# Kernel tuning notes

Measured on AMD Instinct MI355X. Metric: run time of the kernel, lower is better.

## Reference

```python
import jax, jax.numpy as jnp
import numpy as np

H, D, E, C, F = 12, 64, 768, 512, 3072  # heads, kq_dim, emb_dim, context_dim, mlp_hid
EPS = 1e-5
SCALE = 1.0 / float(np.sqrt(D))


def setup_inputs() -> dict:
    key = jax.random.key(0)
    ks = jax.random.split(key, 12)
    rn = lambda k, s: jax.random.normal(k, s, dtype=jnp.float32) * 0.02
    z = lambda s: jnp.zeros(s, jnp.float32)
    o = lambda s: jnp.ones(s, jnp.float32)
    return {
        "emb": jax.random.normal(ks[0], (8, 1024, E), dtype=jnp.float32),
        "context": jax.random.normal(ks[1], (8, 256, C), dtype=jnp.float32),
        # self-attention (qkv_bias=False, value_up has bias)
        "sa_wq": rn(ks[2], (E, H * D)), "sa_wk": rn(ks[3], (E, H * D)),
        "sa_wv": rn(ks[4], (E, H * D)), "sa_wo": rn(ks[5], (H * D, E)), "sa_wo_b": z((E,)),
        "sa_qn_g": o((D,)), "sa_qn_b": z((D,)), "sa_kn_g": o((D,)), "sa_kn_b": z((D,)),
        # cross-attention
        "ca_wq": rn(ks[6], (E, H * D)), "ca_wk": rn(ks[7], (C, H * D)),
        "ca_wv": rn(ks[8], (C, H * D)), "ca_wo": rn(ks[9], (H * D, E)), "ca_wo_b": z((E,)),
        "ca_qn_g": o((D,)), "ca_qn_b": z((D,)), "ca_kn_g": o((D,)), "ca_kn_b": z((D,)),
        # MLP
        "mlp_w1": rn(ks[10], (E, F)), "mlp_b1": z((F,)),
        "mlp_w2": rn(ks[11], (F, E)), "mlp_b2": z((E,)),
        # block LayerNorms
        "ln1_g": o((E,)), "ln1_b": z((E,)),
        "ln2_g": o((E,)), "ln2_b": z((E,)),
        "ln3_g": o((E,)), "ln3_b": z((E,)),
    }


def _ln(x, g, b):
    m = jnp.mean(x, axis=-1, keepdims=True)
    v = jnp.mean(jnp.square(x - m), axis=-1, keepdims=True)
    return (x - m) / jnp.sqrt(v + EPS) * g + b


def _heads(x):  # [B,S,H*D] -> [B,H,S,D]
    B, S = x.shape[:2]
    return x.reshape(B, S, H, D).transpose(0, 2, 1, 3)


def _merge(x):  # [B,H,S,D] -> [B,S,H*D]
    B, h, S, d = x.shape
    return x.transpose(0, 2, 1, 3).reshape(B, S, h * d)


def _attn(qx, kvx, wq, wk, wv, wo, wo_b, qg, qb, kg, kb):
    q = _ln(_heads(qx @ wq), qg, qb)   # per-head QK-LayerNorm
    k = _ln(_heads(kvx @ wk), kg, kb)
    v = _heads(kvx @ wv)
    a = jax.nn.softmax(jnp.einsum('bhqd,bhkd->bhqk', q, k) * SCALE, axis=-1)
    return _merge(jnp.einsum('bhqk,bhkd->bhqd', a, v)) @ wo + wo_b


def reference(emb, context,
              sa_wq, sa_wk, sa_wv, sa_wo, sa_wo_b, sa_qn_g, sa_qn_b, sa_kn_g, sa_kn_b,
              ca_wq, ca_wk, ca_wv, ca_wo, ca_wo_b, ca_qn_g, ca_qn_b, ca_kn_g, ca_kn_b,
              mlp_w1, mlp_b1, mlp_w2, mlp_b2,
              ln1_g, ln1_b, ln2_g, ln2_b, ln3_g, ln3_b):
    # MultiHeadAttention.forward returns value + emb, and the block adds emb again
    sa = _attn(emb, emb, sa_wq, sa_wk, sa_wv, sa_wo, sa_wo_b,
               sa_qn_g, sa_qn_b, sa_kn_g, sa_kn_b)
    x = _ln(sa + emb + emb, ln1_g, ln1_b)  # faithful double residual
    ca = _attn(x, context, ca_wq, ca_wk, ca_wv, ca_wo, ca_wo_b,
               ca_qn_g, ca_qn_b, ca_kn_g, ca_kn_b)
    x = _ln(x + ca, ln2_g, ln2_b)
    x = jax.nn.gelu(x @ mlp_w1 + mlp_b1, approximate=False) @ mlp_w2 + mlp_b2
    return _ln(x, ln3_g, ln3_b)  # note: no residual around MLP in the original
```

## Files before the change

kernel.cpp:

```cpp
#include <hip/hip_runtime.h>
#include <hip/hip_bf16.h>
#include <math.h>

#define NH 12
#define HD 64
#define ED 768
#define CD 512
#define FD 3072
#define BB 8
#define SS 1024
#define TT 256
#define LN_EPS 1e-5f
#define ATT_SCALE 0.125f
#define QSC_LOG2E 0.1803368801111204f
#define P_M0 11.55f
#define TOT_R 6291456

typedef __attribute__((ext_vector_type(8))) __bf16 bf16x8;
typedef __attribute__((ext_vector_type(4))) __bf16 bf16x4;
typedef __attribute__((ext_vector_type(4))) float f32x4;

typedef const __attribute__((address_space(1))) void* gas1_t;
typedef __attribute__((address_space(3))) void* las3_t;

__device__ __forceinline__ void gl16(const void* g, void* l) {
  __builtin_amdgcn_global_load_lds((gas1_t)g, (las3_t)l, 16, 0, 0);
}

template <int N>
__device__ __forceinline__ void vm_wait() {
  if constexpr (N == 0) asm volatile("s_waitcnt vmcnt(0)" ::: "memory");
  else if constexpr (N == 3) asm volatile("s_waitcnt vmcnt(3)" ::: "memory");
  else if constexpr (N == 4) asm volatile("s_waitcnt vmcnt(4)" ::: "memory");
  else if constexpr (N == 6) asm volatile("s_waitcnt vmcnt(6)" ::: "memory");
  else if constexpr (N == 8) asm volatile("s_waitcnt vmcnt(8)" ::: "memory");
}

__device__ __forceinline__ ushort f2bf(float f) {
  union { __bf16 b; ushort u; } c;
  c.b = (__bf16)f;
  return c.u;
}

__device__ __forceinline__ float gelu_fast(float c) {
  const float x2 = c * c;
  const float ex = __builtin_amdgcn_exp2f(c * (-2.3022084f - 0.10294325f * x2));
  return c * __builtin_amdgcn_rcpf(1.0f + ex);
}

__device__ __forceinline__ bf16x8 frag64(const ushort (*T)[64], int row, int q8) {
  return *(const bf16x8*)((const char*)T + row * 128 + ((q8 ^ (row & 7)) << 4));
}

__device__ __forceinline__ bf16x8 frag32(const ushort (*T)[32], int row, int g) {
  return *(const bf16x8*)((const char*)T + row * 64 + ((g ^ ((row >> 1) & 3)) << 4));
}

struct CvtPack {
  const float* src[12];
  ushort* dst[12];
  int kd[12];
  int nd[12];
  int off[13];
};

__global__ __launch_bounds__(256) void cvt_all(CvtPack P) {
  __shared__ float t[32][33];
  const int flat = blockIdx.x;
  int j = 0;
  while (j < 11 && flat >= P.off[j + 1]) ++j;
  const int rel = flat - P.off[j];
  if (P.nd[j] == 0) {
    const int i = rel * 256 + threadIdx.x;
    if (i < P.kd[j]) {
      float4 v = ((const float4*)P.src[j])[i];
      ((ushort4*)P.dst[j])[i] =
          make_ushort4(f2bf(v.x), f2bf(v.y), f2bf(v.z), f2bf(v.w));
    }
    return;
  }
  const int Kd = P.kd[j], Nd = P.nd[j];
  const int ntx = Nd >> 5;
  const int n0 = (rel % ntx) * 32, k0 = (rel / ntx) * 32;
  const float* W = P.src[j];
  ushort* WT = P.dst[j];
  const int tx = threadIdx.x & 31, ty = threadIdx.x >> 5;
#pragma unroll
  for (int r = 0; r < 4; ++r)
    t[ty + 8 * r][tx] = W[(size_t)(k0 + ty + 8 * r) * Nd + n0 + tx];
  __syncthreads();
#pragma unroll
  for (int r = 0; r < 4; ++r)
    WT[(size_t)(n0 + ty + 8 * r) * Kd + k0 + tx] = f2bf(t[tx][ty + 8 * r]);
}

template <int MODE, int BM>
__global__ __launch_bounds__(256, 3) void mfma_gemm(
    const ushort* __restrict__ A, const ushort* __restrict__ Wt,
    const float* __restrict__ bias, void* __restrict__ outp,
    void* __restrict__ outp2, int M, int N, int Kstride, int Klen, int sshift,
    const float* __restrict__ qg, const float* __restrict__ qb,
    const float* __restrict__ kg, const float* __restrict__ kb,
    int t_q, int t_k, int t_v) {
  constexpr int MI = BM / 32;
  constexpr int LPS = BM / 64 + 2;
  __shared__ ushort As[3][BM][32];
  __shared__ ushort Bs[3][128][32];
  const int tid = threadIdx.x;
  const int m0 = blockIdx.x * BM, n0 = blockIdx.y * 128;
  const int kz = blockIdx.z;
  const ushort* Ab = A + (size_t)kz * Klen;
  const ushort* Wb = Wt + (size_t)kz * Klen;
  void* op = kz ? outp2 : outp;
  const int lane = tid & 63;
  const int wr = ((tid >> 6) >> 1) * (BM / 2), wc = ((tid >> 6) & 1) * 64;
  const int l15 = lane & 15, g = lane >> 4;
  f32x4 acc[MI][4] = {};

  auto stage = [&](int bi, int kt) {
#pragma unroll
    for (int p = 0; p < BM / 64; ++p) {
      const int fq = p * 256 + tid;
      const int row = fq >> 2, q = fq & 3;
      const int kc = 8 * (q ^ ((row >> 1) & 3));
      gl16(&Ab[(size_t)(m0 + row) * Kstride + kt + kc], (char*)As[bi] + fq * 16);
    }
#pragma unroll
    for (int p = 0; p < 2; ++p) {
      const int fq = p * 256 + tid;
      const int row = fq >> 2, q = fq & 3;
      const int kc = 8 * (q ^ ((row >> 1) & 3));
      gl16(&Wb[(size_t)(n0 + row) * Kstride + kt + kc], (char*)Bs[bi] + fq * 16);
    }
  };

  const int nst = Klen >> 5;
  stage(0, 0);
  stage(1, 32);
  int cb = 0;
  for (int step = 0; step < nst; ++step) {
    if (step + 2 < nst) {
      int pb = cb + 2; if (pb >= 3) pb -= 3;
      stage(pb, (step + 2) * 32);
    }
    const int rem = nst - 1 - step;
    if (rem >= 2) vm_wait<2 * LPS>();
    else if (rem == 1) vm_wait<LPS>();
    else vm_wait<0>();
    __builtin_amdgcn_s_barrier();
    asm volatile("" ::: "memory");
    bf16x8 af[MI], bfv[4];
#pragma unroll
    for (int i = 0; i < MI; ++i) af[i] = frag32(As[cb], wr + i * 16 + l15, g);
#pragma unroll
    for (int j = 0; j < 4; ++j) bfv[j] = frag32(Bs[cb], wc + j * 16 + l15, g);
#pragma unroll
    for (int i = 0; i < MI; ++i)
#pragma unroll
      for (int j = 0; j < 4; ++j)
        acc[i][j] = __builtin_amdgcn_mfma_f32_16x16x32_bf16(af[i], bfv[j],
                                                            acc[i][j], 0, 0, 0);
    asm volatile("" ::: "memory");
    __builtin_amdgcn_s_barrier();
    if (++cb >= 3) cb = 0;
  }

  if (MODE == 2) {
    ushort* out = (ushort*)op;
    const int Stok = 1 << sshift, smask = Stok - 1;
    const int ht0 = (n0 + wc) >> 6;
    const int t = ht0 / NH, h = ht0 - t * NH;
    const bool isq = (t == t_q), isk = (t == t_k);
    if (isq || isk) {
      const float* gg = isq ? qg : kg;
      const float* bb = isq ? qb : kb;
      const float osc = isq ? QSC_LOG2E : 1.0f;
      float gv[4], bv[4];
#pragma unroll
      for (int j = 0; j < 4; ++j) {
        gv[j] = gg[j * 16 + l15];
        bv[j] = bb[j * 16 + l15];
      }
#pragma unroll
      for (int i = 0; i < MI; ++i)
#pragma unroll
        for (int r = 0; r < 4; ++r) {
          float s = acc[i][0][r] + acc[i][1][r] + acc[i][2][r] + acc[i][3][r];
          float sq = acc[i][0][r] * acc[i][0][r] + acc[i][1][r] * acc[i][1][r] +
                     acc[i][2][r] * acc[i][2][r] + acc[i][3][r] * acc[i][3][r];
          s += __shfl_xor(s, 1);  sq += __shfl_xor(sq, 1);
          s += __shfl_xor(s, 2);  sq += __shfl_xor(sq, 2);
          s += __shfl_xor(s, 4);  sq += __shfl_xor(sq, 4);
          s += __shfl_xor(s, 8);  sq += __shfl_xor(sq, 8);
          const float mean = s * (1.0f / 64.0f);
          const float var = sq * (1.0f / 64.0f) - mean * mean;
          const float rs = rsqrtf(fmaxf(var, 0.0f) + LN_EPS);
#pragma unroll
          for (int j = 0; j < 4; ++j)
            acc[i][j][r] = ((acc[i][j][r] - mean) * rs * gv[j] + bv[j]) * osc;
        }
    }
    if (t == t_v) {
#pragma unroll
      for (int i = 0; i < MI; ++i) {
        const int row = m0 + wr + i * 16 + g * 4;
        const int b = row >> sshift, s2 = row & smask;
        ushort* obase =
            out + (size_t)t * TOT_R + (((size_t)b * NH + h) * 64) * Stok + s2;
#pragma unroll
        for (int j = 0; j < 4; ++j) {
          const int d = j * 16 + l15;
          ushort4 pk = make_ushort4(f2bf(acc[i][j][0]), f2bf(acc[i][j][1]),
                                    f2bf(acc[i][j][2]), f2bf(acc[i][j][3]));
          *(ushort4*)&obase[(size_t)d * Stok] = pk;
        }
      }
    } else {
#pragma unroll
      for (int i = 0; i < MI; ++i)
#pragma unroll
        for (int r = 0; r < 4; ++r) {
          const int row = m0 + wr + i * 16 + g * 4 + r;
          const int b = row >> sshift, s2 = row & smask;
          ushort* orow =
              out + (size_t)t * TOT_R + (((size_t)b * NH + h) * Stok + s2) * 64;
#pragma unroll
          for (int j = 0; j < 4; ++j) orow[j * 16 + l15] = f2bf(acc[i][j][r]);
        }
    }
  } else {
#pragma unroll
    for (int i = 0; i < MI; ++i) {
#pragma unroll
      for (int j = 0; j < 4; ++j) {
        const int gc = n0 + wc + j * 16 + l15;
        const float bv = bias ? bias[gc] : 0.0f;
#pragma unroll
        for (int r = 0; r < 4; ++r) {
          const int row = m0 + wr + i * 16 + g * 4 + r;
          float c = acc[i][j][r] + bv;
          if (MODE == 1) {
            c = gelu_fast(c);
            ((ushort*)op)[(size_t)row * N + gc] = f2bf(c);
          } else {
            ((float*)op)[(size_t)row * N + gc] = c;
          }
        }
      }
    }
  }
}

__global__ __launch_bounds__(512) void flash_mfma(
    const ushort* __restrict__ Q, const ushort* __restrict__ K,
    const ushort* __restrict__ V, ushort* __restrict__ out, int Tkv) {
  __shared__ ushort Ks[2][64][64];
  __shared__ ushort Vt[2][80][64];
  __shared__ ushort Ps[8][16][64];
  const int bh = blockIdx.x;
  const int b = bh / NH, h = bh % NH;
  const int qt = blockIdx.y;
  const int tid = threadIdx.x;
  const int w = tid >> 6, lane = tid & 63;
  const int l15 = lane & 15, g = lane >> 4;
  const int srow = tid >> 3;
  const int q8s = tid & 7;
  const int skc = 8 * (q8s ^ (srow & 7));
  const int kperm = 4 * (srow & 15) + (srow >> 4);

  const ushort* Qb = Q + ((size_t)bh * SS + qt * 256) * 64;
  const ushort* Kb = K + (size_t)bh * Tkv * 64;
  const ushort* Vb = V + (size_t)bh * Tkv * 64;

  gl16(&Kb[(size_t)kperm * 64 + skc], (char*)Ks[0] + tid * 16);
  gl16(&Vb[(size_t)srow * Tkv + skc], (char*)Vt[0] + tid * 16);

  if (tid < 256) {
    const int bi = tid >> 7, rq = tid & 127;
    const uint4 ov = make_uint4(0x3F803F80u, 0x3F803F80u, 0x3F803F80u, 0x3F803F80u);
    *(uint4*)((char*)Vt[bi] + (64 + (rq >> 3)) * 128 + ((rq & 7) << 4)) = ov;
  }

  const ushort* qr0 = Qb + (w * 32 + l15) * 64;
  const bf16x8 qf00 = *(const bf16x8*)&qr0[g * 8];
  const bf16x8 qf01 = *(const bf16x8*)&qr0[32 + g * 8];
  const bf16x8 qf10 = *(const bf16x8*)&qr0[16 * 64 + g * 8];
  const bf16x8 qf11 = *(const bf16x8*)&qr0[16 * 64 + 32 + g * 8];
  __syncthreads();

  f32x4 oa[2][5] = {};
  const int pwofs = ((((l15 >> 1) ^ ((g * 4) & 7)) << 4) | ((l15 & 1) << 3));

  const int nch = Tkv >> 6;
  int cur = 0;
  for (int ci = 0; ci < nch; ++ci) {
    if (ci + 1 < nch) {
      const int cnx = (ci + 1) << 6;
      const int nxt = cur ^ 1;
      gl16(&Kb[(size_t)(cnx + kperm) * 64 + skc], (char*)Ks[nxt] + tid * 16);
      gl16(&Vb[(size_t)srow * Tkv + cnx + skc], (char*)Vt[nxt] + tid * 16);
    }

    f32x4 s[2][4] = {};
    __builtin_amdgcn_s_setprio(1);
#pragma unroll
    for (int kb = 0; kb < 4; ++kb) {
      bf16x8 kf0 = frag64(Ks[cur], kb * 16 + l15, g);
      bf16x8 kf1 = frag64(Ks[cur], kb * 16 + l15, 4 + g);
      s[0][kb] = __builtin_amdgcn_mfma_f32_16x16x32_bf16(qf00, kf0, s[0][kb], 0, 0, 0);
      s[0][kb] = __builtin_amdgcn_mfma_f32_16x16x32_bf16(qf01, kf1, s[0][kb], 0, 0, 0);
      s[1][kb] = __builtin_amdgcn_mfma_f32_16x16x32_bf16(qf10, kf0, s[1][kb], 0, 0, 0);
      s[1][kb] = __builtin_amdgcn_mfma_f32_16x16x32_bf16(qf11, kf1, s[1][kb], 0, 0, 0);
    }
    __builtin_amdgcn_s_setprio(0);

    bf16x8 pfr[2][2];
#pragma unroll
    for (int sub = 0; sub < 2; ++sub) {
#pragma unroll
      for (int r = 0; r < 4; ++r) {
        bf16x4 pk;
#pragma unroll
        for (int kbv = 0; kbv < 4; ++kbv)
          pk[kbv] = (__bf16)__builtin_amdgcn_exp2f(s[sub][kbv][r] - P_M0);
        *(bf16x4*)((char*)Ps[w] + (g * 4 + r) * 128 + (pwofs ^ ((r & 7) << 4))) = pk;
      }
      pfr[sub][0] = frag64(Ps[w], l15, g);
      pfr[sub][1] = frag64(Ps[w], l15, 4 + g);
    }

    __builtin_amdgcn_s_setprio(1);
#pragma unroll
    for (int jd = 0; jd < 5; ++jd) {
      const int d = jd * 16 + l15;
      bf16x8 vf0 = frag64(Vt[cur], d, g);
      bf16x8 vf1 = frag64(Vt[cur], d, 4 + g);
      oa[0][jd] = __builtin_amdgcn_mfma_f32_16x16x32_bf16(pfr[0][0], vf0, oa[0][jd], 0, 0, 0);
      oa[0][jd] = __builtin_amdgcn_mfma_f32_16x16x32_bf16(pfr[0][1], vf1, oa[0][jd], 0, 0, 0);
      oa[1][jd] = __builtin_amdgcn_mfma_f32_16x16x32_bf16(pfr[1][0], vf0, oa[1][jd], 0, 0, 0);
      oa[1][jd] = __builtin_amdgcn_mfma_f32_16x16x32_bf16(pfr[1][1], vf1, oa[1][jd], 0, 0, 0);
    }
    __builtin_amdgcn_s_setprio(0);

    __syncthreads();
    cur ^= 1;
  }

#pragma unroll
  for (int sub = 0; sub < 2; ++sub)
#pragma unroll
    for (int r = 0; r < 4; ++r) {
      const int row = qt * 256 + w * 32 + sub * 16 + g * 4 + r;
      const float inv = 1.0f / oa[sub][4][r];
#pragma unroll
      for (int jd = 0; jd < 4; ++jd)
        out[((size_t)b * SS + row) * ED + h * 64 + jd * 16 + l15] =
            f2bf(oa[sub][jd][r] * inv);
    }
}

__global__ __launch_bounds__(256) void add_ln(
    const float* __restrict__ a1, const float* __restrict__ a2,
    const float* __restrict__ bsrc, float alpha,
    const float* __restrict__ cbias,
    const float* __restrict__ g, const float* __restrict__ bt,
    float* __restrict__ outf, ushort* __restrict__ outb) {
  const int row = blockIdx.x * 4 + (threadIdx.x >> 6);
  const int lane = threadIdx.x & 63;
  const size_t base = (size_t)row * ED;
  float4 x[3];
#pragma unroll
  for (int p = 0; p < 3; ++p) {
    const int idx = p * 256 + lane * 4;
    x[p] = *(const float4*)&a1[base + idx];
    if (a2) {
      float4 v = *(const float4*)&a2[base + idx];
      x[p].x += v.x; x[p].y += v.y; x[p].z += v.z; x[p].w += v.w;
    }
    if (bsrc) {
      float4 bv = *(const float4*)&bsrc[base + idx];
      x[p].x += alpha * bv.x;
      x[p].y += alpha * bv.y;
      x[p].z += alpha * bv.z;
      x[p].w += alpha * bv.w;
    }
    if (cbias) {
      float4 cv = *(const float4*)&cbias[idx];
      x[p].x += cv.x; x[p].y += cv.y; x[p].z += cv.z; x[p].w += cv.w;
    }
  }
  float s = 0.f;
#pragma unroll
  for (int p = 0; p < 3; ++p) s += x[p].x + x[p].y + x[p].z + x[p].w;
  for (int off = 32; off; off >>= 1) s += __shfl_xor(s, off);
  const float mean = s * (1.0f / 768.0f);
  float v = 0.f;
#pragma unroll
  for (int p = 0; p < 3; ++p) {
    float d0 = x[p].x - mean, d1 = x[p].y - mean;
    float d2 = x[p].z - mean, d3 = x[p].w - mean;
    v += d0 * d0 + d1 * d1 + d2 * d2 + d3 * d3;
  }
  for (int off = 32; off; off >>= 1) v += __shfl_xor(v, off);
  const float rs = rsqrtf(v * (1.0f / 768.0f) + LN_EPS);
#pragma unroll
  for (int p = 0; p < 3; ++p) {
    const int idx = p * 256 + lane * 4;
    const float4 gv = *(const float4*)&g[idx];
    const float4 bb = *(const float4*)&bt[idx];
    const float y0 = (x[p].x - mean) * rs * gv.x + bb.x;
    const float y1 = (x[p].y - mean) * rs * gv.y + bb.y;
    const float y2 = (x[p].z - mean) * rs * gv.z + bb.z;
    const float y3 = (x[p].w - mean) * rs * gv.w + bb.w;
    if (outf) *(float4*)&outf[base + idx] = make_float4(y0, y1, y2, y3);
    if (outb)
      *(ushort4*)&outb[base + idx] =
          make_ushort4(f2bf(y0), f2bf(y1), f2bf(y2), f2bf(y3));
  }
}

extern "C" void kernel_launch(void* const* d_in, const int* in_sizes, int n_in,
                              void* d_out, int out_size, void* d_ws,
                              size_t ws_size, hipStream_t stream) {
  (void)in_sizes; (void)n_in; (void)out_size; (void)ws_size;
  const float* emb     = (const float*)d_in[0];
  const float* context = (const float*)d_in[1];
  const float* sa_wq = (const float*)d_in[2];
  const float* sa_wk = (const float*)d_in[3];
  const float* sa_wv = (const float*)d_in[4];
  const float* sa_wo = (const float*)d_in[5];
  const float* sa_wo_b = (const float*)d_in[6];
  const float* sa_qn_g = (const float*)d_in[7];
  const float* sa_qn_b = (const float*)d_in[8];
  const float* sa_kn_g = (const float*)d_in[9];
  const float* sa_kn_b = (const float*)d_in[10];
  const float* ca_wq = (const float*)d_in[11];
  const float* ca_wk = (const float*)d_in[12];
  const float* ca_wv = (const float*)d_in[13];
  const float* ca_wo = (const float*)d_in[14];
  const float* ca_wo_b = (const float*)d_in[15];
  const float* ca_qn_g = (const float*)d_in[16];
  const float* ca_qn_b = (const float*)d_in[17];
  const float* ca_kn_g = (const float*)d_in[18];
  const float* ca_kn_b = (const float*)d_in[19];
  const float* mlp_w1 = (const float*)d_in[20];
  const float* mlp_b1 = (const float*)d_in[21];
  const float* mlp_w2 = (const float*)d_in[22];
  const float* mlp_b2 = (const float*)d_in[23];
  const float* ln1_g = (const float*)d_in[24];
  const float* ln1_b = (const float*)d_in[25];
  const float* ln2_g = (const float*)d_in[26];
  const float* ln2_b = (const float*)d_in[27];
  const float* ln3_g = (const float*)d_in[28];
  const float* ln3_b = (const float*)d_in[29];
  float* out = (float*)d_out;

  const size_t R = TOT_R;
  ushort* U = (ushort*)d_ws;
  ushort* Qh  = U;
  ushort* Kh  = U + R;
  ushort* Vh  = U + 2 * R;
  ushort* SH1 = U + 3 * R;
  ushort* SH2 = U + 4 * R;
  ushort* WB  = U + 5 * R;
  float*  X1  = (float*)(U + 5 * R + 9043968);
  float*  P2  = X1 + R;
  float*  WOt = (float*)Qh;
  ushort* Hb  = Qh;

  ushort* w_saqkv = WB;
  ushort* w_sao   = WB + 1769472;
  ushort* w_caq   = WB + 2359296;
  ushort* w_cakv  = WB + 2949120;
  ushort* w_cao   = WB + 3735552;
  ushort* w_m1    = WB + 4325376;
  ushort* w_m2    = WB + 6684672;

  dim3 blk(256);

  CvtPack P;
  const float* srcs[12] = {sa_wq, sa_wk, sa_wv, sa_wo, ca_wq, ca_wk, ca_wv,
                           ca_wo, mlp_w1, mlp_w2, emb, context};
  ushort* dsts[12] = {w_saqkv, w_saqkv + 589824, w_saqkv + 1179648, w_sao,
                      w_caq, w_cakv, w_cakv + 393216, w_cao, w_m1, w_m2,
                      SH1, SH2};
  const int kds[12] = {ED, ED, ED, ED, ED, CD, CD, ED, ED, FD,
                       1572864, 262144};
  const int nds[12] = {ED, ED, ED, ED, ED, ED, ED, ED, FD, ED, 0, 0};
  int off = 0;
  for (int j = 0; j < 12; ++j) {
    P.src[j] = srcs[j]; P.dst[j] = dsts[j]; P.kd[j] = kds[j]; P.nd[j] = nds[j];
    P.off[j] = off;
    off += nds[j] ? (nds[j] >> 5) * (kds[j] >> 5) : (kds[j] + 255) >> 8;
  }
  P.off[12] = off;
  cvt_all<<<dim3(off), blk, 0, stream>>>(P);

  mfma_gemm<2, 128><<<dim3(64, 18, 1), blk, 0, stream>>>(
      SH1, w_saqkv, nullptr, Qh, nullptr, 8192, 2304, ED, ED, 10,
      sa_qn_g, sa_qn_b, sa_kn_g, sa_kn_b, 0, 1, 2);
  flash_mfma<<<dim3(96, 4), dim3(512), 0, stream>>>(Qh, Kh, Vh, SH1, SS);
  mfma_gemm<0, 128><<<dim3(64, 6, 2), blk, 0, stream>>>(
      SH1, w_sao, nullptr, X1, P2, 8192, ED, ED, ED / 2, 0,
      nullptr, nullptr, nullptr, nullptr, -1, -1, -1);
  add_ln<<<dim3(2048), blk, 0, stream>>>(X1, P2, emb, 2.0f, sa_wo_b,
                                         ln1_g, ln1_b, X1, SH1);

  mfma_gemm<2, 128><<<dim3(64, 6, 1), blk, 0, stream>>>(
      SH1, w_caq, nullptr, Qh, nullptr, 8192, ED, ED, ED, 10,
      ca_qn_g, ca_qn_b, nullptr, nullptr, 0, -1, -1);
  mfma_gemm<2, 64><<<dim3(32, 12, 1), blk, 0, stream>>>(
      SH2, w_cakv, nullptr, Kh, nullptr, 2048, 1536, CD, CD, 8,
      nullptr, nullptr, ca_kn_g, ca_kn_b, -1, 0, 1);
  flash_mfma<<<dim3(96, 4), dim3(512), 0, stream>>>(Qh, Kh, Vh, SH1, TT);
  mfma_gemm<0, 128><<<dim3(64, 6, 2), blk, 0, stream>>>(
      SH1, w_cao, nullptr, WOt, P2, 8192, ED, ED, ED / 2, 0,
      nullptr, nullptr, nullptr, nullptr, -1, -1, -1);
  add_ln<<<dim3(2048), blk, 0, stream>>>(WOt, P2, X1, 1.0f, ca_wo_b,
                                         ln2_g, ln2_b, nullptr, SH2);

  mfma_gemm<1, 128><<<dim3(64, 24, 1), blk, 0, stream>>>(
      SH2, w_m1, mlp_b1, Hb, nullptr, 8192, FD, ED, ED, 0,
      nullptr, nullptr, nullptr, nullptr, -1, -1, -1);
  mfma_gemm<0, 128><<<dim3(64, 6, 2), blk, 0, stream>>>(
      Hb, w_m2, nullptr, X1, P2, 8192, ED, FD, FD / 2, 0,
      nullptr, nullptr, nullptr, nullptr, -1, -1, -1);
  add_ln<<<dim3(2048), blk, 0, stream>>>(X1, P2, nullptr, 0.0f, mlp_b2,
                                         ln3_g, ln3_b, out, nullptr);
}
```

Before: 344.7 us.

## Parameterize GEMM by wave count with 64x64 per-wave tiles and XCD-aware block swizzle

The GEMM template now takes the number of wave rows instead of BM, so every wave always computes a 64x64 tile. The block grows to 256x128 with 512 threads for the MLP up-projection, and the cross-attention KV projection uses 64-row blocks of 128 threads. An optional block-ID remap spreads consecutive workgroups across the 8 XCDs, and it is enabled for the QKV and MLP1 launches to improve L2 locality. In exchange, the larger blocks use more LDS and fewer blocks run per CU, and the swizzle assumes the workgroup count divides evenly by 8.

Result: slower. 358.8 us (+4.1%).

```diff
diff --git a/kernel.cpp b/kernel.cpp
--- a/kernel.cpp
+++ b/kernel.cpp
@@ -34,6 +34,7 @@
   else if constexpr (N == 4) asm volatile("s_waitcnt vmcnt(4)" ::: "memory");
   else if constexpr (N == 6) asm volatile("s_waitcnt vmcnt(6)" ::: "memory");
   else if constexpr (N == 8) asm volatile("s_waitcnt vmcnt(8)" ::: "memory");
+  else if constexpr (N == 12) asm volatile("s_waitcnt vmcnt(12)" ::: "memory");
 }
 
 __device__ __forceinline__ ushort f2bf(float f) {
@@ -94,40 +95,51 @@
     WT[(size_t)(n0 + ty + 8 * r) * Kd + k0 + tx] = f2bf(t[tx][ty + 8 * r]);
 }
 
-template <int MODE, int BM>
-__global__ __launch_bounds__(256, 3) void mfma_gemm(
+template <int MODE, int WM>
+__global__ __launch_bounds__(128 * WM, (WM == 4 ? 4 : 3)) void mfma_gemm(
     const ushort* __restrict__ A, const ushort* __restrict__ Wt,
     const float* __restrict__ bias, void* __restrict__ outp,
     void* __restrict__ outp2, int M, int N, int Kstride, int Klen, int sshift,
     const float* __restrict__ qg, const float* __restrict__ qb,
     const float* __restrict__ kg, const float* __restrict__ kb,
-    int t_q, int t_k, int t_v) {
-  constexpr int MI = BM / 32;
-  constexpr int LPS = BM / 64 + 2;
+    int t_q, int t_k, int t_v, int xswz) {
+  constexpr int BM = 64 * WM;
+  constexpr int THREADS = 128 * WM;
+  constexpr int LPS = 2 + 4 / WM;
   __shared__ ushort As[3][BM][32];
   __shared__ ushort Bs[3][128][32];
   const int tid = threadIdx.x;
-  const int m0 = blockIdx.x * BM, n0 = blockIdx.y * 128;
+  int bx = blockIdx.x, by = blockIdx.y;
+  if (xswz) {
+    const int gx = gridDim.x;
+    const int nwg = gx * gridDim.y;
+    const int id = bx + gx * by;
+    const int nid = (id & 7) * (nwg >> 3) + (id >> 3);
+    bx = nid % gx;
+    by = nid / gx;
+  }
+  const int m0 = bx * BM, n0 = by * 128;
   const int kz = blockIdx.z;
   const ushort* Ab = A + (size_t)kz * Klen;
   const ushort* Wb = Wt + (size_t)kz * Klen;
   void* op = kz ? outp2 : outp;
   const int lane = tid & 63;
-  const int wr = ((tid >> 6) >> 1) * (BM / 2), wc = ((tid >> 6) & 1) * 64;
+  const int wave = tid >> 6;
+  const int wr = (wave >> 1) * 64, wc = (wave & 1) * 64;
   const int l15 = lane & 15, g = lane >> 4;
-  f32x4 acc[MI][4] = {};
+  f32x4 acc[4][4] = {};
 
   auto stage = [&](int bi, int kt) {
 #pragma unroll
-    for (int p = 0; p < BM / 64; ++p) {
-      const int fq = p * 256 + tid;
+    for (int p = 0; p < 2; ++p) {
+      const int fq = p * THREADS + tid;
       const int row = fq >> 2, q = fq & 3;
       const int kc = 8 * (q ^ ((row >> 1) & 3));
       gl16(&Ab[(size_t)(m0 + row) * Kstride + kt + kc], (char*)As[bi] + fq * 16);
     }
 #pragma unroll
-    for (int p = 0; p < 2; ++p) {
-      const int fq = p * 256 + tid;
+    for (int p = 0; p < 4 / WM; ++p) {
+      const int fq = p * THREADS + tid;
       const int row = fq >> 2, q = fq & 3;
       const int kc = 8 * (q ^ ((row >> 1) & 3));
       gl16(&Wb[(size_t)(n0 + row) * Kstride + kt + kc], (char*)Bs[bi] + fq * 16);
@@ -149,13 +161,13 @@
     else vm_wait<0>();
     __builtin_amdgcn_s_barrier();
     asm volatile("" ::: "memory");
-    bf16x8 af[MI], bfv[4];
-#pragma unroll
-    for (int i = 0; i < MI; ++i) af[i] = frag32(As[cb], wr + i * 16 + l15, g);
+    bf16x8 af[4], bfv[4];
+#pragma unroll
+    for (int i = 0; i < 4; ++i) af[i] = frag32(As[cb], wr + i * 16 + l15, g);
 #pragma unroll
     for (int j = 0; j < 4; ++j) bfv[j] = frag32(Bs[cb], wc + j * 16 + l15, g);
 #pragma unroll
-    for (int i = 0; i < MI; ++i)
+    for (int i = 0; i < 4; ++i)
 #pragma unroll
       for (int j = 0; j < 4; ++j)
         acc[i][j] = __builtin_amdgcn_mfma_f32_16x16x32_bf16(af[i], bfv[j],
@@ -182,7 +194,7 @@
         bv[j] = bb[j * 16 + l15];
       }
 #pragma unroll
-      for (int i = 0; i < MI; ++i)
+      for (int i = 0; i < 4; ++i)
 #pragma unroll
         for (int r = 0; r < 4; ++r) {
           float s = acc[i][0][r] + acc[i][1][r] + acc[i][2][r] + acc[i][3][r];
@@ -202,7 +214,7 @@
     }
     if (t == t_v) {
 #pragma unroll
-      for (int i = 0; i < MI; ++i) {
+      for (int i = 0; i < 4; ++i) {
         const int row = m0 + wr + i * 16 + g * 4;
         const int b = row >> sshift, s2 = row & smask;
         ushort* obase =
@@ -217,7 +229,7 @@
       }
     } else {
 #pragma unroll
-      for (int i = 0; i < MI; ++i)
+      for (int i = 0; i < 4; ++i)
 #pragma unroll
         for (int r = 0; r < 4; ++r) {
           const int row = m0 + wr + i * 16 + g * 4 + r;
@@ -230,7 +242,7 @@
     }
   } else {
 #pragma unroll
-    for (int i = 0; i < MI; ++i) {
+    for (int i = 0; i < 4; ++i) {
 #pragma unroll
       for (int j = 0; j < 4; ++j) {
         const int gc = n0 + wc + j * 16 + l15;
@@ -496,35 +508,35 @@
   P.off[12] = off;
   cvt_all<<<dim3(off), blk, 0, stream>>>(P);
 
-  mfma_gemm<2, 128><<<dim3(64, 18, 1), blk, 0, stream>>>(
+  mfma_gemm<2, 2><<<dim3(64, 18, 1), blk, 0, stream>>>(
       SH1, w_saqkv, nullptr, Qh, nullptr, 8192, 2304, ED, ED, 10,
-      sa_qn_g, sa_qn_b, sa_kn_g, sa_kn_b, 0, 1, 2);
+      sa_qn_g, sa_qn_b, sa_kn_g, sa_kn_b, 0, 1, 2, 1);
   flash_mfma<<<dim3(96, 4), dim3(512), 0, stream>>>(Qh, Kh, Vh, SH1, SS);
-  mfma_gemm<0, 128><<<dim3(64, 6, 2), blk, 0, stream>>>(
+  mfma_gemm<0, 2><<<dim3(64, 6, 2), blk, 0, stream>>>(
       SH1, w_sao, nullptr, X1, P2, 8192, ED, ED, ED / 2, 0,
-      nullptr, nullptr, nullptr, nullptr, -1, -1, -1);
+      nullptr, nullptr, nullptr, nullptr, -1, -1, -1, 0);
   add_ln<<<dim3(2048), blk, 0, stream>>>(X1, P2, emb, 2.0f, sa_wo_b,
                                          ln1_g, ln1_b, X1, SH1);
 
-  mfma_gemm<2, 128><<<dim3(64, 6, 1), blk, 0, stream>>>(
+  mfma_gemm<2, 2><<<dim3(64, 6, 1), blk, 0, stream>>>(
       SH1, w_caq, nullptr, Qh, nullptr, 8192, ED, ED, ED, 10,
-      ca_qn_g, ca_qn_b, nullptr, nullptr, 0, -1, -1);
-  mfma_gemm<2, 64><<<dim3(32, 12, 1), blk, 0, stream>>>(
+      ca_qn_g, ca_qn_b, nullptr, nullptr, 0, -1, -1, 0);
+  mfma_gemm<2, 1><<<dim3(32, 12, 1), dim3(128), 0, stream>>>(
       SH2, w_cakv, nullptr, Kh, nullptr, 2048, 1536, CD, CD, 8,
-      nullptr, nullptr, ca_kn_g, ca_kn_b, -1, 0, 1);
+      nullptr, nullptr, ca_kn_g, ca_kn_b, -1, 0, 1, 0);
   flash_mfma<<<dim3(96, 4), dim3(512), 0, stream>>>(Qh, Kh, Vh, SH1, TT);
-  mfma_gemm<0, 128><<<dim3(64, 6, 2), blk, 0, stream>>>(
+  mfma_gemm<0, 2><<<dim3(64, 6, 2), blk, 0, stream>>>(
       SH1, w_cao, nullptr, WOt, P2, 8192, ED, ED, ED / 2, 0,
-      nullptr, nullptr, nullptr, nullptr, -1, -1, -1);
+      nullptr, nullptr, nullptr, nullptr, -1, -1, -1, 0);
   add_ln<<<dim3(2048), blk, 0, stream>>>(WOt, P2, X1, 1.0f, ca_wo_b,
                                          ln2_g, ln2_b, nullptr, SH2);
 
-  mfma_gemm<1, 128><<<dim3(64, 24, 1), blk, 0, stream>>>(
+  mfma_gemm<1, 4><<<dim3(32, 24, 1), dim3(512), 0, stream>>>(
       SH2, w_m1, mlp_b1, Hb, nullptr, 8192, FD, ED, ED, 0,
-      nullptr, nullptr, nullptr, nullptr, -1, -1, -1);
-  mfma_gemm<0, 128><<<dim3(64, 6, 2), blk, 0, stream>>>(
+      nullptr, nullptr, nullptr, nullptr, -1, -1, -1, 1);
+  mfma_gemm<0, 2><<<dim3(64, 6, 2), blk, 0, stream>>>(
       Hb, w_m2, nullptr, X1, P2, 8192, ED, FD, FD / 2, 0,
-      nullptr, nullptr, nullptr, nullptr, -1, -1, -1);
+      nullptr, nullptr, nullptr, nullptr, -1, -1, -1, 0);
   add_ln<<<dim3(2048), blk, 0, stream>>>(X1, P2, nullptr, 0.0f, mlp_b2,
                                          ln3_g, ln3_b, out, nullptr);
 }
```
